# Performance work log

Measured on AMD Instinct MI355X. Metric: run time of the kernel, lower is better.

## Reference

```python
import jax, jax.numpy as jnp
import numpy as np

B, T, C = 4, 2048, 1024
H = 16
HD = C // H  # 64


def setup_inputs() -> dict:
    key = jax.random.key(0)
    k1, k2, k3 = jax.random.split(key, 3)
    x = jax.random.normal(k1, (B, T, C), dtype=jnp.float32)
    W_attn = jax.random.normal(k2, (C, 3 * C), dtype=jnp.float32) * (1.0 / np.sqrt(C))
    b_attn = jnp.zeros((3 * C,), dtype=jnp.float32)
    W_proj = jax.random.normal(k3, (C, C), dtype=jnp.float32) * (1.0 / np.sqrt(C))
    b_proj = jnp.zeros((C,), dtype=jnp.float32)
    return {"x": x, "W_attn": W_attn, "b_attn": b_attn, "W_proj": W_proj, "b_proj": b_proj}


def reference(x, W_attn, b_attn, W_proj, b_proj):
    Bx, Tx, Cx = x.shape
    qkv = x @ W_attn + b_attn                      # [B,T,3C]
    q, k, v = jnp.split(qkv, 3, axis=-1)
    # [B,T,C] -> [B,H,T,HD]
    q = q.reshape(Bx, Tx, H, HD).transpose(0, 2, 1, 3)
    k = k.reshape(Bx, Tx, H, HD).transpose(0, 2, 1, 3)
    v = v.reshape(Bx, Tx, H, HD).transpose(0, 2, 1, 3)
    att = jnp.einsum('bhqd,bhkd->bhqk', q, k) / jnp.sqrt(jnp.float32(HD))
    causal = jnp.tril(jnp.ones((Tx, Tx), dtype=bool))
    att = jnp.where(causal[None, None], att, -jnp.inf)
    att = jax.nn.softmax(att, axis=-1)
    y = jnp.einsum('bhqk,bhkd->bhqd', att, v)      # [B,H,T,HD]
    y = y.transpose(0, 2, 1, 3).reshape(Bx, Tx, Cx)
    return y @ W_proj + b_proj
```

## Files before the change

### kernel.cpp

```cpp
#include <hip/hip_runtime.h>
#include <hip/hip_bf16.h>

typedef unsigned short u16;
typedef __attribute__((ext_vector_type(8))) short bf16x8;
typedef __attribute__((ext_vector_type(4))) float f32x4;

#define MFMA16(a, b, c) __builtin_amdgcn_mfma_f32_16x16x32_bf16((a), (b), (c), 0, 0, 0)

__device__ __forceinline__ u16 f2bf(float f) {
  union { float f; unsigned u; } v; v.f = f;
  unsigned r = v.u + 0x7fffu + ((v.u >> 16) & 1u);
  return (u16)(r >> 16);
}

__device__ __forceinline__ unsigned pk_trunc(float hi, float lo) {
  union { float f; unsigned u; } a, b; a.f = hi; b.f = lo;
  return __builtin_amdgcn_perm(a.u, b.u, 0x07060302u);
}

__device__ __forceinline__ void gload_lds16(const u16* g, u16* l) {
  __builtin_amdgcn_global_load_lds((const __attribute__((address_space(1))) void*)g,
                                   (__attribute__((address_space(3))) void*)l, 16, 0, 0);
}

__global__ __launch_bounds__(256) void convert_bf16_k(const float* __restrict__ in,
                                                      u16* __restrict__ out, int n) {
  int i = (blockIdx.x * 256 + threadIdx.x) * 8;
  if (i >= n) return;
  float4 v0 = *(const float4*)(in + i);
  float4 v1 = *(const float4*)(in + i + 4);
  uint4 o;
  o.x = (unsigned)f2bf(v0.x) | ((unsigned)f2bf(v0.y) << 16);
  o.y = (unsigned)f2bf(v0.z) | ((unsigned)f2bf(v0.w) << 16);
  o.z = (unsigned)f2bf(v1.x) | ((unsigned)f2bf(v1.y) << 16);
  o.w = (unsigned)f2bf(v1.z) | ((unsigned)f2bf(v1.w) << 16);
  *(uint4*)(out + i) = o;
}

__global__ __launch_bounds__(256) void transpose2_k(const float* __restrict__ Wa, u16* __restrict__ WaT,
                                                    const float* __restrict__ Wp, u16* __restrict__ WpT) {
  __shared__ float tile[64][65];
  int b = blockIdx.x;
  const float* W; u16* Wt; int N, n0, k0;
  if (b < 768) { W = Wa; Wt = WaT; N = 3072; n0 = (b % 48) * 64; k0 = (b / 48) * 64; }
  else { int c = b - 768; W = Wp; Wt = WpT; N = 1024; n0 = (c & 15) * 64; k0 = (c >> 4) * 64; }
  const int tx = threadIdx.x & 63, ty = threadIdx.x >> 6;
#pragma unroll
  for (int i = 0; i < 16; ++i)
    tile[ty + 4 * i][tx] = W[(size_t)(k0 + ty + 4 * i) * N + n0 + tx];
  __syncthreads();
#pragma unroll
  for (int i = 0; i < 16; ++i)
    Wt[(size_t)(n0 + ty + 4 * i) * 1024 + k0 + tx] = f2bf(tile[tx][ty + 4 * i]);
}

#define BAR() asm volatile("s_barrier" ::: "memory")
#define WLG()                                                   \
  do {                                                          \
    asm volatile("s_waitcnt lgkmcnt(0)" ::: "memory");          \
    __builtin_amdgcn_sched_barrier(0);                          \
  } while (0)
#define VMW(N) asm volatile("s_waitcnt vmcnt(" #N ")" ::: "memory")

__global__ __launch_bounds__(256, 2) void gemm_qkv_cr(const u16* __restrict__ A,
                                                      const u16* __restrict__ Bt,
                                                      const float* __restrict__ bias,
                                                      u16* __restrict__ Qo, u16* __restrict__ Ko,
                                                      u16* __restrict__ Vt) {
  __shared__ u16 sm[3][12288];
  const int bid = blockIdx.x;
  const int swz = (bid & 7) * 96 + (bid >> 3);
  const int m0 = (swz / 12) * 128, n0 = (swz % 12) * 256;
  const int tid = threadIdx.x, w = tid >> 6, lane = tid & 63;
  const int fr = lane & 15, fg = lane >> 4;
  const int sk = (tid & 1) * 8 + ((((tid >> 1) ^ (tid >> 5)) & 1) << 4);
  const int lsw = fr * 32 + ((fg * 8) ^ ((fr & 8) ? 16 : 0));
  const int aoff = lsw;
  const int boff = 4096 + w * 2048 + lsw;

  const u16* gA = A + (size_t)(m0 + (tid >> 2)) * 1024 + sk;
  const u16* gB = Bt + (size_t)(n0 + (tid >> 2)) * 1024 + sk;

#define QSTG_A(SL, C) \
  gload_lds16(gA + (size_t)(C) * 65536 + kofs, &sm[SL][(C) * 2048 + tid * 8])
#define QSTG_B(SL, C) \
  gload_lds16(gB + (size_t)(C) * 65536 + kofs, &sm[SL][4096 + (C) * 2048 + tid * 8])

  f32x4 acc[8][4];
#pragma unroll
  for (int i = 0; i < 8; ++i)
#pragma unroll
    for (int j = 0; j < 4; ++j) acc[i][j] = (f32x4){0, 0, 0, 0};

  int kofs = 0;
  QSTG_A(0, 0); QSTG_A(0, 1);
  QSTG_B(0, 0); QSTG_B(0, 1); QSTG_B(0, 2); QSTG_B(0, 3);
  kofs = 32;
  QSTG_A(1, 0); QSTG_A(1, 1);
  QSTG_B(1, 0); QSTG_B(1, 1); QSTG_B(1, 2); QSTG_B(1, 3);
  kofs = 64;
  VMW(6); BAR();

#define QLD_A(SL, M0_)                                                    \
  _Pragma("unroll") for (int i = 0; i < 4; ++i)                           \
      av[i] = *(const bf16x8*)&sm[SL][aoff + ((M0_) + i) * 512];
#define QLD_B(SL)                                                         \
  _Pragma("unroll") for (int i = 0; i < 4; ++i)                           \
      bv[i] = *(const bf16x8*)&sm[SL][boff + i * 512];
#define QMM(MB0)                                                          \
  __builtin_amdgcn_s_setprio(1);                                          \
  _Pragma("unroll") for (int i = 0; i < 4; ++i)                           \
      _Pragma("unroll") for (int j = 0; j < 4; ++j)                       \
          acc[(MB0) + i][j] = MFMA16(av[i], bv[j], acc[(MB0) + i][j]);    \
  __builtin_amdgcn_s_setprio(0);

#define QTILE(SL, SS, STG, CHK)                                                \
  {                                                                            \
    bf16x8 av[4], bv[4];                                                       \
    if (STG) { QSTG_A(SS, 0); QSTG_A(SS, 1);                                   \
               QSTG_B(SS, 0); QSTG_B(SS, 1); QSTG_B(SS, 2); QSTG_B(SS, 3); }   \
    QLD_A(SL, 0) QLD_B(SL)                                                     \
    WLG(); QMM(0)                                                              \
    QLD_A(SL, 4)                                                               \
    WLG(); QMM(4)                                                              \
    CHK;                                                                       \
    BAR();                                                                     \
    kofs += 32;                                                                \
  }

#pragma unroll 1
  for (int tp = 0; tp < 10; ++tp) {
    QTILE(0, 2, 1, VMW(6)) QTILE(1, 0, 1, VMW(6)) QTILE(2, 1, 1, VMW(6))
  }
  QTILE(0, 0, 0, VMW(0))
  QTILE(1, 0, 0, (void)0)

  const int which = n0 >> 10;
  if (which == 2) {
#pragma unroll
    for (int nb = 0; nb < 4; ++nb) {
      const int n = n0 + w * 64 + nb * 16 + fr;
      const float bs = bias[n];
      const int c = n & 1023, h = c >> 6, hd = c & 63;
#pragma unroll
      for (int mb = 0; mb < 8; ++mb) {
        const int mbase = m0 + mb * 16 + fg * 4;
        const int bb = mbase >> 11;
        const int tt = mbase & 2047;
        ushort4 pv;
        pv.x = f2bf(acc[mb][nb][0] + bs);
        pv.y = f2bf(acc[mb][nb][1] + bs);
        pv.z = f2bf(acc[mb][nb][2] + bs);
        pv.w = f2bf(acc[mb][nb][3] + bs);
        *(ushort4*)(Vt + ((size_t)(bb * 16 + h) * 64 + hd) * 2048 + tt) = pv;
      }
    }
  } else {
    u16* buf = &sm[0][0];
    const float sc = (which == 0) ? 0.125f : 1.0f;
    u16* outp = (which == 0) ? Qo : Ko;
    float bs4[4];
#pragma unroll
    for (int nb = 0; nb < 4; ++nb) bs4[nb] = bias[n0 + w * 64 + nb * 16 + fr];
#pragma unroll
    for (int mb = 0; mb < 8; ++mb) {
#pragma unroll
      for (int nb = 0; nb < 4; ++nb) {
#pragma unroll
        for (int r = 0; r < 4; ++r) {
          const int rl = mb * 16 + fg * 4 + r;
          const int col = (w * 64 + nb * 16 + fr) ^ ((rl & 7) << 3);
          buf[rl * 256 + col] = f2bf((acc[mb][nb][r] + bs4[nb]) * sc);
        }
      }
    }
    BAR();
#pragma unroll
    for (int p2 = 0; p2 < 2; ++p2) {
      const int rl = p2 * 64 + (tid >> 2), c4 = (tid & 3) * 64;
      const int m = m0 + rl;
      const int bb = m >> 11, tt = m & 2047;
      const int n = n0 + c4;
      const int h = (n & 1023) >> 6;
      u16* dst = outp + ((size_t)(bb * 16 + h) * 2048 + tt) * 64;
#pragma unroll
      for (int i = 0; i < 8; ++i) {
        const int col = (c4 + i * 8) ^ ((rl & 7) << 3);
        *(uint4*)(dst + i * 8) = *(const uint4*)&buf[rl * 256 + col];
      }
    }
  }
#undef QSTG_A
#undef QSTG_B
#undef QLD_A
#undef QLD_B
#undef QMM
#undef QTILE
}

#define RING_LANE_CONSTS                                                    \
  const int tid = threadIdx.x, w = tid >> 6, lane = tid & 63;               \
  const int wm = w >> 2, wn = w & 3;                                        \
  const int fr = lane & 15, fg = lane >> 4;                                 \
  const int sr = lane >> 2;                                                 \
  const int sk = (lane & 1) * 8 + ((((lane >> 1) ^ (lane >> 5)) & 1) << 4); \
  const int lsw = fr * 32 + ((fg * 8) ^ ((fr & 8) ? 16 : 0));

__global__ __launch_bounds__(512, 2) void gemm_proj_r4(const u16* __restrict__ A,
                                                       const u16* __restrict__ Bt,
                                                       const float* __restrict__ bias,
                                                       float* __restrict__ O) {
  __shared__ u16 sm[4][12288];
  const int bid = blockIdx.x;
  const int swz = (bid & 7) * 32 + (bid >> 3);
  const int m0 = (swz >> 3) * 256, n0 = (swz & 7) * 128;
  RING_LANE_CONSTS
  const int aoff = wm * 4096 + lsw;
  const int boff = 8192 + wn * 1024 + lsw;

  const u16* gAw = A + (size_t)(m0 + sr) * 1024 + sk + (size_t)w * 16384;
  const u16* gBw = Bt + (size_t)(n0 + sr) * 1024 + sk + (size_t)w * 16384;

#define PSTG_A(SL, C, KO) \
  gload_lds16(gAw + (size_t)(C) * 131072 + (KO), &sm[SL][(C) * 4096 + w * 512 + lane * 8])
#define PSTG_B(SL, KO) \
  gload_lds16(gBw + (KO), &sm[SL][8192 + w * 512 + lane * 8])

  f32x4 acc[8][2];
#pragma unroll
  for (int i = 0; i < 8; ++i)
#pragma unroll
    for (int j = 0; j < 2; ++j) acc[i][j] = (f32x4){0, 0, 0, 0};

  PSTG_A(0, 0, 0);  PSTG_B(0, 0);  PSTG_A(0, 1, 0);
  PSTG_A(1, 0, 32); PSTG_B(1, 32); PSTG_A(1, 1, 32);
  PSTG_A(2, 0, 64); PSTG_B(2, 64); PSTG_A(2, 1, 64);
  int kofs = 96;
  VMW(6); BAR();

#define PLD_A(SL, M0_)                                                    \
  _Pragma("unroll") for (int i = 0; i < 4; ++i)                           \
      av[i] = *(const bf16x8*)&sm[SL][aoff + ((M0_) + i) * 512];
#define PLD_B(SL)                                                         \
  _Pragma("unroll") for (int i = 0; i < 2; ++i)                           \
      bv[i] = *(const bf16x8*)&sm[SL][boff + i * 512];
#define PMM(MB0)                                                          \
  __builtin_amdgcn_s_setprio(1);                                          \
  _Pragma("unroll") for (int i = 0; i < 4; ++i)                           \
      _Pragma("unroll") for (int j = 0; j < 2; ++j)                       \
          acc[(MB0) + i][j] = MFMA16(av[i], bv[j], acc[(MB0) + i][j]);    \
  __builtin_amdgcn_s_setprio(0);

#define PTILE(SL, SS, STG, CHK)                                                \
  {                                                                            \
    bf16x8 av[4], bv[2];                                                       \
    if (STG) { PSTG_A(SS, 0, kofs); PSTG_B(SS, kofs); PSTG_A(SS, 1, kofs); }   \
    PLD_A(SL, 0) PLD_B(SL)                                                     \
    WLG(); PMM(0)                                                              \
    PLD_A(SL, 4)                                                               \
    WLG(); PMM(4)                                                              \
    CHK;                                                                       \
    BAR();                                                                     \
    kofs += 32;                                                                \
  }

#pragma unroll 1
  for (int tp = 0; tp < 7; ++tp) {
    PTILE(0, 3, 1, VMW(6)) PTILE(1, 0, 1, VMW(6)) PTILE(2, 1, 1, VMW(6)) PTILE(3, 2, 1, VMW(6))
  }
  PTILE(0, 3, 1, VMW(6))
  PTILE(1, 0, 0, VMW(3))
  PTILE(2, 0, 0, VMW(0))
  PTILE(3, 0, 0, (void)0)

#pragma unroll
  for (int nb = 0; nb < 2; ++nb) {
    const int n = n0 + wn * 32 + nb * 16 + fr;
    const float bs = bias[n];
#pragma unroll
    for (int mb = 0; mb < 8; ++mb) {
      const int tg = m0 + wm * 128 + mb * 16 + fg * 4;
#pragma unroll
      for (int r = 0; r < 4; ++r) O[(size_t)(tg + r) * 1024 + n] = acc[mb][nb][r] + bs;
    }
  }
#undef PSTG_A
#undef PSTG_B
#undef PLD_A
#undef PLD_B
#undef PMM
#undef PTILE
}

#define PSTR 72
__global__ __launch_bounds__(256) void attn_k(const u16* __restrict__ Q,
                                              const u16* __restrict__ Kb,
                                              const u16* __restrict__ Vt,
                                              u16* __restrict__ Y) {
  __shared__ u16 Ks[64 * 72];
  __shared__ u16 Vs[64 * 72];
  __shared__ u16 Ps[4 * 32 * PSTR];
  const int L = blockIdx.x;
  const int xcd = L & 7, slot = L >> 3;
  const int bh = xcd * 8 + (slot & 7);
  const int i2 = slot >> 3;
  const int qt = (i2 & 4) ? ((i2 & 8) ? 4 + (i2 & 3) : (i2 & 3))
                          : ((i2 & 8) ? 11 - (i2 & 3) : 15 - (i2 & 3));
  const int tid = threadIdx.x, w = tid >> 6, lane = tid & 63;
  const int fr = lane & 15, fg = lane >> 4;
  const u16* Qp = Q + (size_t)bh * 2048 * 64;
  const u16* Kp = Kb + (size_t)bh * 2048 * 64;
  const u16* Vp = Vt + (size_t)bh * 64 * 2048;
  const int qw = qt * 128 + w * 32;

  bf16x8 qa[2][2];
#pragma unroll
  for (int g = 0; g < 2; ++g)
#pragma unroll
    for (int c = 0; c < 2; ++c)
      qa[g][c] = *(const bf16x8*)(Qp + (size_t)(qw + g * 16 + fr) * 64 + c * 32 + fg * 8);

  float li[2] = {0.f, 0.f};
  f32x4 ot[2][4];
#pragma unroll
  for (int g = 0; g < 2; ++g)
#pragma unroll
    for (int mb = 0; mb < 4; ++mb) ot[g][mb] = (f32x4){0, 0, 0, 0};

  const int srow = tid >> 2, scol = (tid & 3) * 16;
  u16* Pw = Ps + w * 32 * PSTR;
  const int nk = 2 * qt + 2;
  const u16* Kg = Kp + (size_t)srow * 64 + scol;
  const u16* Vg = Vp + (size_t)srow * 2048 + scol;

  uint4 kr0 = *(const uint4*)(Kg);
  uint4 kr1 = *(const uint4*)(Kg + 8);
  uint4 vr0 = *(const uint4*)(Vg);
  uint4 vr1 = *(const uint4*)(Vg + 8);

  for (int jt = 0; jt < nk; ++jt) {
    const int k0 = jt * 64;
    if (jt) __syncthreads();
    *(uint4*)&Ks[srow * 72 + scol] = kr0;
    *(uint4*)&Ks[srow * 72 + scol + 8] = kr1;
    *(uint4*)&Vs[srow * 72 + scol] = vr0;
    *(uint4*)&Vs[srow * 72 + scol + 8] = vr1;
    __syncthreads();
    if (jt + 1 < nk) {
      const int kn = (jt + 1) * 64;
      kr0 = *(const uint4*)(Kg + (size_t)kn * 64);
      kr1 = *(const uint4*)(Kg + (size_t)kn * 64 + 8);
      vr0 = *(const uint4*)(Vg + kn);
      vr1 = *(const uint4*)(Vg + kn + 8);
    }
    if (k0 > qw + 31) continue;

    bf16x8 kb[4][2];
#pragma unroll
    for (int nb = 0; nb < 4; ++nb) {
      kb[nb][0] = *(const bf16x8*)&Ks[(nb * 16 + fr) * 72 + fg * 8];
      kb[nb][1] = *(const bf16x8*)&Ks[(nb * 16 + fr) * 72 + 32 + fg * 8];
    }
    f32x4 st[2][4];
    __builtin_amdgcn_s_setprio(1);
#pragma unroll
    for (int g = 0; g < 2; ++g)
#pragma unroll
      for (int nb = 0; nb < 4; ++nb) {
        f32x4 z = (f32x4){0, 0, 0, 0};
        z = MFMA16(kb[nb][0], qa[g][0], z);
        z = MFMA16(kb[nb][1], qa[g][1], z);
        st[g][nb] = z;
      }
    __builtin_amdgcn_s_setprio(0);
    const bool needmask = (k0 + 63 > qw);
#pragma unroll
    for (int g = 0; g < 2; ++g) {
      const int q = qw + g * 16 + fr;
      float rs0 = 0.f, rs1 = 0.f;
#pragma unroll
      for (int nb = 0; nb < 4; ++nb) {
        const int kcb = k0 + nb * 16 + 4 * fg;
        float p0 = __expf(st[g][nb][0]);
        float p1 = __expf(st[g][nb][1]);
        float p2 = __expf(st[g][nb][2]);
        float p3 = __expf(st[g][nb][3]);
        if (needmask) {
          p0 = (kcb + 0 > q) ? 0.f : p0;
          p1 = (kcb + 1 > q) ? 0.f : p1;
          p2 = (kcb + 2 > q) ? 0.f : p2;
          p3 = (kcb + 3 > q) ? 0.f : p3;
        }
        rs0 += p0 + p1;
        rs1 += p2 + p3;
        *(uint2*)&Pw[(g * 16 + fr) * PSTR + nb * 16 + 4 * fg] =
            make_uint2(pk_trunc(p1, p0), pk_trunc(p3, p2));
      }
      li[g] += rs0 + rs1;
    }
    bf16x8 pa[2][2];
#pragma unroll
    for (int g = 0; g < 2; ++g)
#pragma unroll
      for (int H = 0; H < 2; ++H)
        pa[g][H] = *(const bf16x8*)&Pw[(g * 16 + fr) * PSTR + H * 32 + fg * 8];
    __builtin_amdgcn_s_setprio(1);
#pragma unroll
    for (int mb = 0; mb < 4; ++mb) {
      bf16x8 vb0 = *(const bf16x8*)&Vs[(mb * 16 + fr) * 72 + fg * 8];
      bf16x8 vb1 = *(const bf16x8*)&Vs[(mb * 16 + fr) * 72 + 32 + fg * 8];
#pragma unroll
      for (int g = 0; g < 2; ++g) {
        ot[g][mb] = MFMA16(vb0, pa[g][0], ot[g][mb]);
        ot[g][mb] = MFMA16(vb1, pa[g][1], ot[g][mb]);
      }
    }
    __builtin_amdgcn_s_setprio(0);
  }

  const int b = bh >> 4, h = bh & 15;
#pragma unroll
  for (int g = 0; g < 2; ++g) {
    float l = li[g];
    l += __shfl_xor(l, 16);
    l += __shfl_xor(l, 32);
    const float inv = 1.0f / l;
    const int t = qw + g * 16 + fr;
    u16* yrow = Y + ((size_t)b * 2048 + t) * 1024 + h * 64;
#pragma unroll
    for (int mb = 0; mb < 4; ++mb) {
      const unsigned d0 = (unsigned)f2bf(ot[g][mb][0] * inv) |
                          ((unsigned)f2bf(ot[g][mb][1] * inv) << 16);
      const unsigned d1 = (unsigned)f2bf(ot[g][mb][2] * inv) |
                          ((unsigned)f2bf(ot[g][mb][3] * inv) << 16);
      *(uint2*)&yrow[mb * 16 + fg * 4] = make_uint2(d0, d1);
    }
  }
}

extern "C" void kernel_launch(void* const* d_in, const int* in_sizes, int n_in,
                              void* d_out, int out_size, void* d_ws, size_t ws_size,
                              hipStream_t stream) {
  const float* x = (const float*)d_in[0];
  const float* Wa = (const float*)d_in[1];
  const float* ba = (const float*)d_in[2];
  const float* Wp = (const float*)d_in[3];
  const float* bp = (const float*)d_in[4];
  float* out = (float*)d_out;

  char* p = (char*)d_ws;
  u16* xb = (u16*)p;   p += (size_t)8192 * 1024 * 2;
  u16* WaT = (u16*)p;  p += (size_t)3072 * 1024 * 2;
  u16* WpT = (u16*)p;  p += (size_t)1024 * 1024 * 2;
  u16* Qb = (u16*)p;   p += (size_t)64 * 2048 * 64 * 2;
  u16* Kbuf = (u16*)p; p += (size_t)64 * 2048 * 64 * 2;
  u16* Vtb = (u16*)p;  p += (size_t)64 * 64 * 2048 * 2;
  u16* Yb = (u16*)p;   p += (size_t)8192 * 1024 * 2;

  convert_bf16_k<<<4096, 256, 0, stream>>>(x, xb, 8192 * 1024);
  transpose2_k<<<1024, 256, 0, stream>>>(Wa, WaT, Wp, WpT);
  gemm_qkv_cr<<<768, 256, 0, stream>>>(xb, WaT, ba, Qb, Kbuf, Vtb);
  attn_k<<<1024, 256, 0, stream>>>(Qb, Kbuf, Vtb, Yb);
  gemm_proj_r4<<<256, 512, 0, stream>>>(Yb, WpT, bp, out);
}
```

Before: 242.9 us.

## Retile output projection GEMM to 128x128 blocks with 3-stage LDS ring

The projection GEMM goes from 256x128 tiles with 512 threads and a 4-slot LDS ring to 128x128 tiles with 256 threads and a 3-slot ring. The grid doubles to 512 blocks so more CUs are busy on this 8192x1024 output, and the smaller LDS footprint should allow more resident blocks. The cost is lower data reuse per tile and a shallower prefetch pipeline, which may expose more global memory latency.

```diff
diff --git a/kernel.cpp b/kernel.cpp
--- a/kernel.cpp
+++ b/kernel.cpp
@@ -198,33 +198,28 @@
 #undef QTILE
 }
 
-#define RING_LANE_CONSTS                                                    \
-  const int tid = threadIdx.x, w = tid >> 6, lane = tid & 63;               \
-  const int wm = w >> 2, wn = w & 3;                                        \
-  const int fr = lane & 15, fg = lane >> 4;                                 \
-  const int sr = lane >> 2;                                                 \
-  const int sk = (lane & 1) * 8 + ((((lane >> 1) ^ (lane >> 5)) & 1) << 4); \
-  const int lsw = fr * 32 + ((fg * 8) ^ ((fr & 8) ? 16 : 0));
-
-__global__ __launch_bounds__(512, 2) void gemm_proj_r4(const u16* __restrict__ A,
+__global__ __launch_bounds__(256, 2) void gemm_proj_cr(const u16* __restrict__ A,
                                                        const u16* __restrict__ Bt,
                                                        const float* __restrict__ bias,
                                                        float* __restrict__ O) {
-  __shared__ u16 sm[4][12288];
+  __shared__ u16 sm[3][8192];
   const int bid = blockIdx.x;
-  const int swz = (bid & 7) * 32 + (bid >> 3);
-  const int m0 = (swz >> 3) * 256, n0 = (swz & 7) * 128;
-  RING_LANE_CONSTS
-  const int aoff = wm * 4096 + lsw;
-  const int boff = 8192 + wn * 1024 + lsw;
-
-  const u16* gAw = A + (size_t)(m0 + sr) * 1024 + sk + (size_t)w * 16384;
-  const u16* gBw = Bt + (size_t)(n0 + sr) * 1024 + sk + (size_t)w * 16384;
-
-#define PSTG_A(SL, C, KO) \
-  gload_lds16(gAw + (size_t)(C) * 131072 + (KO), &sm[SL][(C) * 4096 + w * 512 + lane * 8])
-#define PSTG_B(SL, KO) \
-  gload_lds16(gBw + (KO), &sm[SL][8192 + w * 512 + lane * 8])
+  const int swz = (bid & 7) * 64 + (bid >> 3);
+  const int m0 = (swz >> 3) * 128, n0 = (swz & 7) * 128;
+  const int tid = threadIdx.x, w = tid >> 6, lane = tid & 63;
+  const int fr = lane & 15, fg = lane >> 4;
+  const int sk = (tid & 1) * 8 + ((((tid >> 1) ^ (tid >> 5)) & 1) << 4);
+  const int lsw = fr * 32 + ((fg * 8) ^ ((fr & 8) ? 16 : 0));
+  const int aoff = lsw;
+  const int boff = 4096 + w * 1024 + lsw;
+
+  const u16* gA = A + (size_t)(m0 + (tid >> 2)) * 1024 + sk;
+  const u16* gB = Bt + (size_t)(n0 + (tid >> 2)) * 1024 + sk;
+
+#define PSTG_A(SL, C) \
+  gload_lds16(gA + (size_t)(C) * 65536 + kofs, &sm[SL][(C) * 2048 + tid * 8])
+#define PSTG_B(SL, C) \
+  gload_lds16(gB + (size_t)(C) * 65536 + kofs, &sm[SL][4096 + (C) * 2048 + tid * 8])
 
   f32x4 acc[8][2];
 #pragma unroll
@@ -232,11 +227,12 @@
 #pragma unroll
     for (int j = 0; j < 2; ++j) acc[i][j] = (f32x4){0, 0, 0, 0};
 
-  PSTG_A(0, 0, 0);  PSTG_B(0, 0);  PSTG_A(0, 1, 0);
-  PSTG_A(1, 0, 32); PSTG_B(1, 32); PSTG_A(1, 1, 32);
-  PSTG_A(2, 0, 64); PSTG_B(2, 64); PSTG_A(2, 1, 64);
-  int kofs = 96;
-  VMW(6); BAR();
+  int kofs = 0;
+  PSTG_A(0, 0); PSTG_A(0, 1); PSTG_B(0, 0); PSTG_B(0, 1);
+  kofs = 32;
+  PSTG_A(1, 0); PSTG_A(1, 1); PSTG_B(1, 0); PSTG_B(1, 1);
+  kofs = 64;
+  VMW(4); BAR();
 
 #define PLD_A(SL, M0_)                                                    \
   _Pragma("unroll") for (int i = 0; i < 4; ++i)                           \
@@ -254,7 +250,7 @@
 #define PTILE(SL, SS, STG, CHK)                                                \
   {                                                                            \
     bf16x8 av[4], bv[2];                                                       \
-    if (STG) { PSTG_A(SS, 0, kofs); PSTG_B(SS, kofs); PSTG_A(SS, 1, kofs); }   \
+    if (STG) { PSTG_A(SS, 0); PSTG_A(SS, 1); PSTG_B(SS, 0); PSTG_B(SS, 1); }   \
     PLD_A(SL, 0) PLD_B(SL)                                                     \
     WLG(); PMM(0)                                                              \
     PLD_A(SL, 4)                                                               \
@@ -265,21 +261,19 @@
   }
 
 #pragma unroll 1
-  for (int tp = 0; tp < 7; ++tp) {
-    PTILE(0, 3, 1, VMW(6)) PTILE(1, 0, 1, VMW(6)) PTILE(2, 1, 1, VMW(6)) PTILE(3, 2, 1, VMW(6))
-  }
-  PTILE(0, 3, 1, VMW(6))
-  PTILE(1, 0, 0, VMW(3))
-  PTILE(2, 0, 0, VMW(0))
-  PTILE(3, 0, 0, (void)0)
+  for (int tp = 0; tp < 10; ++tp) {
+    PTILE(0, 2, 1, VMW(4)) PTILE(1, 0, 1, VMW(4)) PTILE(2, 1, 1, VMW(4))
+  }
+  PTILE(0, 0, 0, VMW(0))
+  PTILE(1, 0, 0, (void)0)
 
 #pragma unroll
   for (int nb = 0; nb < 2; ++nb) {
-    const int n = n0 + wn * 32 + nb * 16 + fr;
+    const int n = n0 + w * 32 + nb * 16 + fr;
     const float bs = bias[n];
 #pragma unroll
     for (int mb = 0; mb < 8; ++mb) {
-      const int tg = m0 + wm * 128 + mb * 16 + fg * 4;
+      const int tg = m0 + mb * 16 + fg * 4;
 #pragma unroll
       for (int r = 0; r < 4; ++r) O[(size_t)(tg + r) * 1024 + n] = acc[mb][nb][r] + bs;
     }
@@ -461,5 +455,5 @@
   transpose2_k<<<1024, 256, 0, stream>>>(Wa, WaT, Wp, WpT);
   gemm_qkv_cr<<<768, 256, 0, stream>>>(xb, WaT, ba, Qb, Kbuf, Vtb);
   attn_k<<<1024, 256, 0, stream>>>(Qb, Kbuf, Vtb, Yb);
-  gemm_proj_r4<<<256, 512, 0, stream>>>(Yb, WpT, bp, out);
-}
+  gemm_proj_cr<<<512, 256, 0, stream>>>(Yb, WpT, bp, out);
+}
```

Result: no change. 244.1 us (+0.5%).
